# Performance work log

Measured on AMD Instinct MI355X. Metric: run time of the kernel, lower is better.

Reference implementation:

```python
import jax, jax.numpy as jnp
import numpy as np

B, T, D, S, K = 4, 4096, 1024, 2048, 8

def _l2norm(v, axis=-1, eps=1e-12):
    # matches torch F.normalize: v / max(||v||, eps)
    n = jnp.sqrt(jnp.sum(v * v, axis=axis, keepdims=True))
    return v / jnp.maximum(n, eps)

def setup_inputs() -> dict:
    key = jax.random.key(0)
    ks = jax.random.split(key, 9)
    H = D // 2
    return {
        "x": jax.random.normal(ks[0], (B, T, D), dtype=jnp.float32),
        "memory_keys": jax.random.normal(ks[1], (S, D), dtype=jnp.float32) * 0.02,
        "memory_values": jax.random.normal(ks[2], (S, D), dtype=jnp.float32) * 0.02,
        "Wq": jax.random.normal(ks[3], (D, D), dtype=jnp.float32) * (1.0 / np.sqrt(D)),
        "Wo": jax.random.normal(ks[4], (D, D), dtype=jnp.float32) * (1.0 / np.sqrt(D)),
        "gW1": jax.random.normal(ks[5], (H, 2 * D), dtype=jnp.float32) * (1.0 / np.sqrt(2 * D)),
        "gb1": jnp.zeros((H,), dtype=jnp.float32),
        "gW2": jax.random.normal(ks[6], (1, H), dtype=jnp.float32) * (1.0 / np.sqrt(H)),
        "gb2": jnp.zeros((1,), dtype=jnp.float32),
    }

def reference(x, memory_keys, memory_values, Wq, Wo, gW1, gb1, gW2, gb2):
    # query projection (Linear, no bias): y = x @ W.T
    queries = jnp.einsum('btd,ed->bte', x, Wq)
    keys_norm = _l2norm(memory_keys)          # [S, D]
    queries_norm = _l2norm(queries)           # [B, T, D]
    # cosine similarities [B, T, S]
    sims = jnp.einsum('btd,sd->bts', queries_norm, keys_norm)
    topk_sims, topk_idx = jax.lax.top_k(sims, K)      # [B, T, K]
    topk_w = jax.nn.softmax(topk_sims, axis=-1)       # [B, T, K]
    topk_vals = memory_values[topk_idx]               # [B, T, K, D]
    retrieved = jnp.einsum('btk,btkd->btd', topk_w, topk_vals)
    retrieved = jnp.einsum('btd,ed->bte', retrieved, Wo)
    gate_in = jnp.concatenate([x, retrieved], axis=-1)           # [B, T, 2D]
    h = jax.nn.gelu(jnp.einsum('btc,hc->bth', gate_in, gW1) + gb1, approximate=False)
    gate = jax.nn.sigmoid(jnp.einsum('bth,oh->bto', h, gW2) + gb2)  # [B, T, 1]
    return x + gate * retrieved
```

## Files before the change

### kernel.cpp

```cpp
#include <hip/hip_runtime.h>
#include <math.h>

#define NROWS 16384
#define DDIM  1024
#define SKEYS 2048
#define KTOP  8
#define HDIM  512

typedef short  s16x8 __attribute__((ext_vector_type(8)));
typedef float  f32x4 __attribute__((ext_vector_type(4)));

#define GL16(g, l) __builtin_amdgcn_global_load_lds(                      \
    (const __attribute__((address_space(1))) void*)(g),                   \
    (__attribute__((address_space(3))) void*)(l), 16, 0, 0)

__device__ __forceinline__ float wave_sum(float v) {
#pragma unroll
    for (int off = 32; off > 0; off >>= 1) v += __shfl_xor(v, off, 64);
    return v;
}

__device__ __forceinline__ unsigned short f2bf(float f) {
    union { float f; unsigned u; } c; c.f = f;
    unsigned u = c.u;
    unsigned r = (u + 0x7FFFu + ((u >> 16) & 1u)) >> 16;
    return (unsigned short)r;
}

__device__ __forceinline__ float gelu_exact(float v) {
    return 0.5f * v * (1.0f + erff(v * 0.7071067811865475f));
}

__device__ __forceinline__ ushort4 cvt4(float4 v) {
    ushort4 o;
    o.x = f2bf(v.x); o.y = f2bf(v.y); o.z = f2bf(v.z); o.w = f2bf(v.w);
    return o;
}

__global__ __launch_bounds__(256) void prep_kernel(
        const float* __restrict__ x,   const float* __restrict__ Wq,
        const float* __restrict__ Wo,  const float* __restrict__ mv,
        const float* __restrict__ gW1, const float* __restrict__ mk,
        unsigned short* __restrict__ x_bf, unsigned short* __restrict__ wqcat,
        unsigned short* __restrict__ wo_bf, unsigned short* __restrict__ mv_bf,
        unsigned short* __restrict__ gw1b, unsigned short* __restrict__ kn) {
    int bid = blockIdx.x, t = threadIdx.x;
    {
        float4 v = ((const float4*)(mk + (size_t)bid * DDIM))[t];
        float ss = v.x * v.x + v.y * v.y + v.z * v.z + v.w * v.w;
        ss = wave_sum(ss);
        __shared__ float wsum[4];
        if ((t & 63) == 0) wsum[t >> 6] = ss;
        __syncthreads();
        float tot = wsum[0] + wsum[1] + wsum[2] + wsum[3];
        float sc = 1.0f / fmaxf(sqrtf(tot), 1e-12f);
        float4 o = make_float4(v.x * sc, v.y * sc, v.z * sc, v.w * sc);
        ((ushort4*)(kn + (size_t)bid * DDIM))[t] = cvt4(o);
    }
    int gid = bid * 256 + t, stride = gridDim.x * 256;
    for (int i = gid; i < NROWS * DDIM / 4; i += stride)
        ((ushort4*)x_bf)[i] = cvt4(((const float4*)x)[i]);
    for (int i = gid; i < DDIM * DDIM / 4; i += stride)
        ((ushort4*)wqcat)[i] = cvt4(((const float4*)Wq)[i]);
    for (int i = gid; i < HDIM * 2 * DDIM / 4; i += stride) {
        float4 v = ((const float4*)gW1)[i];
        int r = i >> 9, c4 = i & 511;
        if (c4 < 256) ((ushort4*)wqcat)[DDIM * DDIM / 4 + r * 256 + c4] = cvt4(v);
        else          ((ushort4*)gw1b)[r * 256 + (c4 - 256)] = cvt4(v);
    }
    for (int i = gid; i < DDIM * DDIM / 4; i += stride)
        ((ushort4*)wo_bf)[i] = cvt4(((const float4*)Wo)[i]);
    for (int i = gid; i < SKEYS * DDIM / 4; i += stride)
        ((ushort4*)mv_bf)[i] = cvt4(((const float4*)mv)[i]);
}

template<int MODE, int K0, int KTOT>
__global__ __launch_bounds__(256, 3) void gemm128(
        const unsigned short* __restrict__ A0, const unsigned short* __restrict__ A1,
        const unsigned short* __restrict__ Bm, const float* __restrict__ bias,
        unsigned short* __restrict__ Cb, int Ncols,
        unsigned short* __restrict__ C2, int N2cols, int nsplit) {
    __shared__ __align__(16) unsigned short As[2][4096];
    __shared__ __align__(16) unsigned short Bs[2][4096];

    int tid = threadIdx.x, l = tid & 63, wid = tid >> 6;
    int gx = gridDim.x;
    int nwg = gx * gridDim.y;
    int bid = blockIdx.y * gx + blockIdx.x;
    int cpx = nwg >> 3;
    int sbid = (bid & 7) * cpx + (bid >> 3);
    int m0 = (sbid / gx) * 128;
    int n0 = (sbid % gx) * 128;

    int wr = wid >> 1, wc = wid & 1;
    constexpr int K1 = KTOT - K0;
    constexpr int NT = KTOT >> 5;

    f32x4 acc[4][4];
#pragma unroll
    for (int i = 0; i < 4; ++i)
#pragma unroll
        for (int j = 0; j < 4; ++j) acc[i][j] = (f32x4){0.f, 0.f, 0.f, 0.f};

    int srow   = tid >> 2;
    int schunk = (tid & 3) ^ ((srow >> 1) & 3);
    int offA0[2], offA1[2], offB[2];
#pragma unroll
    for (int i = 0; i < 2; ++i) {
        int ra = m0 + i * 64 + srow;
        offA0[i] = ra * K0;
        offA1[i] = ra * K1;
        offB[i]  = (n0 + i * 64 + srow) * KTOT;
    }
    int ldsU = wid * 512;

#define STAGE(bsel, kt_)                                                       \
    do {                                                                       \
        int gk_ = (kt_) * 32 + schunk * 8;                                     \
        _Pragma("unroll")                                                      \
        for (int i_ = 0; i_ < 2; ++i_) {                                       \
            const unsigned short* ga_ = (K0 == KTOT || gk_ < K0)               \
                ? A0 + offA0[i_] + gk_                                         \
                : A1 + offA1[i_] + (gk_ - K0);                                 \
            GL16(ga_, &As[bsel][i_ * 2048 + ldsU]);                            \
            GL16(Bm + offB[i_] + gk_, &Bs[bsel][i_ * 2048 + ldsU]);            \
        }                                                                      \
    } while (0)

    STAGE(0, 0);

    int frow = l & 15;
    int fp   = (l >> 4) ^ ((frow >> 1) & 3);
    int aoff = (wr * 64 + frow) * 32 + fp * 8;
    int boff = (wc * 64 + frow) * 32 + fp * 8;

#pragma unroll 2
    for (int kt = 0; kt < NT; ++kt) {
        int b = kt & 1;
        if (kt + 1 < NT) {
            STAGE(b ^ 1, kt + 1);
            asm volatile("s_waitcnt vmcnt(4)" ::: "memory");
        } else {
            asm volatile("s_waitcnt vmcnt(0)" ::: "memory");
        }
        __builtin_amdgcn_s_barrier();
        asm volatile("" ::: "memory");

        s16x8 af[4], bfr[4];
#pragma unroll
        for (int mf = 0; mf < 4; ++mf)
            af[mf] = *(const s16x8*)&As[b][aoff + mf * 512];
#pragma unroll
        for (int nf = 0; nf < 4; ++nf)
            bfr[nf] = *(const s16x8*)&Bs[b][boff + nf * 512];

        __builtin_amdgcn_s_setprio(1);
#pragma unroll
        for (int mf = 0; mf < 4; ++mf)
#pragma unroll
            for (int nf = 0; nf < 4; ++nf)
                acc[mf][nf] = __builtin_amdgcn_mfma_f32_16x16x32_bf16(
                    af[mf], bfr[nf], acc[mf][nf], 0, 0, 0);
        __builtin_amdgcn_s_setprio(0);
        asm volatile("" ::: "memory");
        __builtin_amdgcn_s_barrier();
        asm volatile("" ::: "memory");
    }
#undef STAGE

    unsigned short* cptr = Cb;
    int nc = Ncols, cb = n0;
    if (MODE == 2 && n0 >= nsplit) { cptr = C2; nc = N2cols; cb = n0 - nsplit; }

    int crow = (l >> 4) << 2;
    int ccol = l & 15;
#pragma unroll
    for (int mf = 0; mf < 4; ++mf) {
        int gr = m0 + wr * 64 + mf * 16 + crow;
#pragma unroll
        for (int nf = 0; nf < 4; ++nf) {
            int gc = cb + wc * 64 + nf * 16 + ccol;
            f32x4 v = acc[mf][nf];
#pragma unroll
            for (int r2 = 0; r2 < 4; ++r2) {
                unsigned short sv = f2bf(v[r2]);
                if (MODE == 3)
                    sv = sv ^ ((sv & 0x8000) ? 0xFFFFu : 0x8000u);
                cptr[(size_t)(gr + r2) * nc + gc] = sv;
            }
        }
    }
    (void)bias;
}

#define BINS(arr, xk)                                                     \
    do {                                                                  \
        unsigned cur_ = (xk);                                             \
        _Pragma("unroll")                                                 \
        for (int p_ = 0; p_ < 8; ++p_) {                                  \
            unsigned mx_ = arr[p_] > cur_ ? arr[p_] : cur_;               \
            unsigned mn_ = arr[p_] > cur_ ? cur_ : arr[p_];               \
            arr[p_] = mx_; cur_ = mn_;                                    \
        }                                                                 \
    } while (0)

__global__ __launch_bounds__(256) void mega_kernel(
        const unsigned short* __restrict__ q_bf,
        const unsigned short* __restrict__ sims,
        const unsigned short* __restrict__ x_bf,
        const unsigned short* __restrict__ xg1,
        const unsigned short* __restrict__ mvo,
        const unsigned short* __restrict__ mvog,
        const float* __restrict__ gb1, const float* __restrict__ gW2,
        const float* __restrict__ gb2, float* __restrict__ out) {
    int wid = threadIdx.x >> 6, l = threadIdx.x & 63;
    int row = blockIdx.x * 4 + wid;

    const unsigned short* qp = q_bf + (size_t)row * DDIM + l * 16;
    uint4 qa = *(const uint4*)qp, qb = *(const uint4*)(qp + 8);
    unsigned qw[8] = {qa.x, qa.y, qa.z, qa.w, qb.x, qb.y, qb.z, qb.w};
    float ss = 0.f;
#pragma unroll
    for (int j = 0; j < 8; ++j) {
        float lo = __uint_as_float(qw[j] << 16);
        float hi = __uint_as_float(qw[j] & 0xffff0000u);
        ss += lo * lo + hi * hi;
    }
    ss = wave_sum(ss);
    float qs = 1.0f / fmaxf(sqrtf(ss), 1e-12f);

    const unsigned short* sr = sims + (size_t)row * SKEYS;
    unsigned a[8], bb[8];
#pragma unroll
    for (int j = 0; j < 8; ++j) { a[j] = 0u; bb[j] = 0u; }
#pragma unroll
    for (int c = 0; c < 4; ++c) {
        uint4 raw = *(const uint4*)(sr + c * 512 + l * 8);
        unsigned wv[4] = {raw.x, raw.y, raw.z, raw.w};
#pragma unroll
        for (int q2 = 0; q2 < 4; ++q2) {
            unsigned bi0 = (unsigned)(c * 512 + l * 8 + q2 * 2);
            unsigned klo = ((wv[q2] & 0xFFFFu) << 16) | bi0;
            unsigned khi = (wv[q2] & 0xFFFF0000u) | (bi0 + 1);
            if (c < 2) { BINS(a, klo); BINS(a, khi); }
            else       { BINS(bb, klo); BINS(bb, khi); }
        }
    }
#pragma unroll
    for (int j = 0; j < 8; ++j) BINS(a, bb[j]);

    float ov[8]; int oi[8];
#pragma unroll
    for (int j = 0; j < 8; ++j) {
        unsigned best = a[0];
#pragma unroll
        for (int off = 32; off > 0; off >>= 1) {
            unsigned o2 = (unsigned)__shfl_xor((int)best, off, 64);
            best = best > o2 ? best : o2;
        }
        oi[j] = (int)(best & 0xFFFFu);
        unsigned short ks = (unsigned short)(best >> 16);
        unsigned short sv = ks ^ ((ks & 0x8000) ? 0x8000u : 0xFFFFu);
        ov[j] = __uint_as_float(((unsigned)sv) << 16);
        bool hit = (a[0] == best);
#pragma unroll
        for (int p = 0; p < 7; ++p) a[p] = hit ? a[p + 1] : a[p];
        a[7] = hit ? 0u : a[7];
    }

    float w[KTOP];
    float m = ov[0] * qs, ssum = 0.f;
#pragma unroll
    for (int j = 0; j < 8; ++j) { w[j] = expf(ov[j] * qs - m); ssum += w[j]; }
    float sinv = 1.0f / ssum;
#pragma unroll
    for (int j = 0; j < 8; ++j) w[j] *= sinv;

    float r2[16], hp[8];
#pragma unroll
    for (int j = 0; j < 16; ++j) r2[j] = 0.f;
#pragma unroll
    for (int j = 0; j < 8; ++j) hp[j] = 0.f;
#pragma unroll
    for (int k = 0; k < KTOP; ++k) {
        float wk = w[k];
        const unsigned short* mo = mvo + (size_t)oi[k] * DDIM + l * 16;
        uint4 a0 = *(const uint4*)mo;
        uint4 a1 = *(const uint4*)(mo + 8);
        const unsigned short* mg = mvog + (size_t)oi[k] * HDIM + l * 8;
        uint4 g0 = *(const uint4*)mg;
        unsigned aw[8] = {a0.x, a0.y, a0.z, a0.w, a1.x, a1.y, a1.z, a1.w};
#pragma unroll
        for (int j = 0; j < 8; ++j) {
            r2[2 * j]     += wk * __uint_as_float(aw[j] << 16);
            r2[2 * j + 1] += wk * __uint_as_float(aw[j] & 0xffff0000u);
        }
        unsigned gw[4] = {g0.x, g0.y, g0.z, g0.w};
#pragma unroll
        for (int j = 0; j < 4; ++j) {
            hp[2 * j]     += wk * __uint_as_float(gw[j] << 16);
            hp[2 * j + 1] += wk * __uint_as_float(gw[j] & 0xffff0000u);
        }
    }
    uint4 xg = *(const uint4*)(xg1 + (size_t)row * HDIM + l * 8);
    unsigned xgw[4] = {xg.x, xg.y, xg.z, xg.w};
    float p = 0.f;
#pragma unroll
    for (int j = 0; j < 4; ++j) {
        float h0 = gelu_exact(hp[2 * j] + __uint_as_float(xgw[j] << 16)
                              + gb1[l * 8 + 2 * j]);
        float h1 = gelu_exact(hp[2 * j + 1] + __uint_as_float(xgw[j] & 0xffff0000u)
                              + gb1[l * 8 + 2 * j + 1]);
        p += h0 * gW2[l * 8 + 2 * j] + h1 * gW2[l * 8 + 2 * j + 1];
    }
    p = wave_sum(p);
    float gate = 1.0f / (1.0f + expf(-(p + gb2[0])));
    const unsigned short* xr = x_bf + (size_t)row * DDIM + l * 16;
    uint4 x0 = *(const uint4*)xr, x1 = *(const uint4*)(xr + 8);
    unsigned xw[8] = {x0.x, x0.y, x0.z, x0.w, x1.x, x1.y, x1.z, x1.w};
    float o[16];
#pragma unroll
    for (int j = 0; j < 8; ++j) {
        o[2 * j]     = __uint_as_float(xw[j] << 16)         + gate * r2[2 * j];
        o[2 * j + 1] = __uint_as_float(xw[j] & 0xffff0000u) + gate * r2[2 * j + 1];
    }
    float4* po = (float4*)(out + (size_t)row * DDIM + l * 16);
    po[0] = make_float4(o[0], o[1], o[2], o[3]);
    po[1] = make_float4(o[4], o[5], o[6], o[7]);
    po[2] = make_float4(o[8], o[9], o[10], o[11]);
    po[3] = make_float4(o[12], o[13], o[14], o[15]);
}

extern "C" void kernel_launch(void* const* d_in, const int* in_sizes, int n_in,
                              void* d_out, int out_size, void* d_ws, size_t ws_size,
                              hipStream_t stream) {
    (void)in_sizes; (void)n_in; (void)out_size; (void)ws_size;
    const float* x   = (const float*)d_in[0];
    const float* mk  = (const float*)d_in[1];
    const float* mv  = (const float*)d_in[2];
    const float* Wq  = (const float*)d_in[3];
    const float* Wo  = (const float*)d_in[4];
    const float* gW1 = (const float*)d_in[5];
    const float* gb1 = (const float*)d_in[6];
    const float* gW2 = (const float*)d_in[7];
    const float* gb2 = (const float*)d_in[8];
    float* out = (float*)d_out;

    char* w = (char*)d_ws;
    unsigned short* x_bf    = (unsigned short*)w;  w += (size_t)NROWS * DDIM * 2;
    unsigned short* q_bf    = (unsigned short*)w;  w += (size_t)NROWS * DDIM * 2;
    unsigned short* xg1_bf  = (unsigned short*)w;  w += (size_t)NROWS * HDIM * 2;
    unsigned short* kn_bf   = (unsigned short*)w;  w += (size_t)SKEYS * DDIM * 2;
    unsigned short* wqcat   = (unsigned short*)w;  w += (size_t)(DDIM + HDIM) * DDIM * 2;
    unsigned short* gw1b_bf = (unsigned short*)w;  w += (size_t)HDIM * DDIM * 2;
    unsigned short* wo_bf   = (unsigned short*)w;  w += (size_t)DDIM * DDIM * 2;
    unsigned short* mv_bf   = (unsigned short*)w;  w += (size_t)SKEYS * DDIM * 2;
    unsigned short* mvo_bf  = (unsigned short*)w;  w += (size_t)SKEYS * DDIM * 2;
    unsigned short* mvog_bf = (unsigned short*)w;  w += (size_t)SKEYS * HDIM * 2;
    unsigned short* sims    = (unsigned short*)w;  w += (size_t)NROWS * SKEYS * 2;

    prep_kernel<<<SKEYS, 256, 0, stream>>>(x, Wq, Wo, mv, gW1, mk,
                                           x_bf, wqcat, wo_bf, mv_bf, gw1b_bf, kn_bf);

    gemm128<0, DDIM, DDIM><<<dim3(DDIM / 128, SKEYS / 128), 256, 0, stream>>>(
        mv_bf, mv_bf, wo_bf, nullptr, mvo_bf, DDIM, nullptr, 0, 0);

    gemm128<0, DDIM, DDIM><<<dim3(HDIM / 128, SKEYS / 128), 256, 0, stream>>>(
        mvo_bf, mvo_bf, gw1b_bf, nullptr, mvog_bf, HDIM, nullptr, 0, 0);

    gemm128<2, DDIM, DDIM><<<dim3((DDIM + HDIM) / 128, NROWS / 128), 256, 0, stream>>>(
        x_bf, x_bf, wqcat, nullptr, q_bf, DDIM, xg1_bf, HDIM, DDIM);

    gemm128<3, DDIM, DDIM><<<dim3(SKEYS / 128, NROWS / 128), 256, 0, stream>>>(
        q_bf, q_bf, kn_bf, nullptr, sims, SKEYS, nullptr, 0, 0);

    mega_kernel<<<NROWS / 4, 256, 0, stream>>>(
        q_bf, sims, x_bf, xg1_bf, mvo_bf, mvog_bf, gb1, gW2, gb2, out);
}
```

Measured before the change: 299.5 us.

## Merge independent GEMMs into dual-problem launches and fuse query norm into epilogue

The four separate GEMM launches are replaced by two launches of a runtime-parameterised dual GEMM kernel. Each launch pairs a large GEMM with a small independent one (query/gate-projection with memory-values@Wo, sims with mvo@gW1b), so the small problems fill tail waves instead of running as their own underfilled grids. The query GEMM epilogue also accumulates per-row squared norms via shuffles and atomics into a workspace buffer. The mega kernel then reads one float per row instead of re-reading the full bf16 query row. This adds a memset, atomics, and runtime mode branches in place of compile-time templates. The norm is now computed from fp32 accumulators rather than rounded bf16 values.

```diff
diff --git a/kernel.cpp b/kernel.cpp
--- a/kernel.cpp
+++ b/kernel.cpp
@@ -74,27 +74,30 @@
         ((ushort4*)mv_bf)[i] = cvt4(((const float4*)mv)[i]);
 }
 
-template<int MODE, int K0, int KTOT>
-__global__ __launch_bounds__(256, 3) void gemm128(
-        const unsigned short* __restrict__ A0, const unsigned short* __restrict__ A1,
-        const unsigned short* __restrict__ Bm, const float* __restrict__ bias,
-        unsigned short* __restrict__ Cb, int Ncols,
-        unsigned short* __restrict__ C2, int N2cols, int nsplit) {
+struct GArg {
+    const unsigned short* A;
+    const unsigned short* B;
+    unsigned short* C;
+    unsigned short* C2;
+    float* qinv;
+    int Ncols, N2cols, nsplit, gx, nblocks, mode;
+};
+
+__global__ __launch_bounds__(256, 3) void dualgemm(GArg g0, GArg g1, int split) {
     __shared__ __align__(16) unsigned short As[2][4096];
     __shared__ __align__(16) unsigned short Bs[2][4096];
 
     int tid = threadIdx.x, l = tid & 63, wid = tid >> 6;
-    int gx = gridDim.x;
-    int nwg = gx * gridDim.y;
-    int bid = blockIdx.y * gx + blockIdx.x;
-    int cpx = nwg >> 3;
+    bool first = ((int)blockIdx.x < split);
+    GArg g = first ? g0 : g1;
+    int bid = first ? blockIdx.x : blockIdx.x - split;
+    int cpx = g.nblocks >> 3;
     int sbid = (bid & 7) * cpx + (bid >> 3);
-    int m0 = (sbid / gx) * 128;
-    int n0 = (sbid % gx) * 128;
+    int m0 = (sbid / g.gx) * 128;
+    int n0 = (sbid % g.gx) * 128;
 
     int wr = wid >> 1, wc = wid & 1;
-    constexpr int K1 = KTOT - K0;
-    constexpr int NT = KTOT >> 5;
+    constexpr int NT = 32;
 
     f32x4 acc[4][4];
 #pragma unroll
@@ -104,13 +107,11 @@
 
     int srow   = tid >> 2;
     int schunk = (tid & 3) ^ ((srow >> 1) & 3);
-    int offA0[2], offA1[2], offB[2];
+    int offA[2], offB[2];
 #pragma unroll
     for (int i = 0; i < 2; ++i) {
-        int ra = m0 + i * 64 + srow;
-        offA0[i] = ra * K0;
-        offA1[i] = ra * K1;
-        offB[i]  = (n0 + i * 64 + srow) * KTOT;
+        offA[i] = (m0 + i * 64 + srow) * 1024;
+        offB[i] = (n0 + i * 64 + srow) * 1024;
     }
     int ldsU = wid * 512;
 
@@ -119,11 +120,8 @@
         int gk_ = (kt_) * 32 + schunk * 8;                                     \
         _Pragma("unroll")                                                      \
         for (int i_ = 0; i_ < 2; ++i_) {                                       \
-            const unsigned short* ga_ = (K0 == KTOT || gk_ < K0)               \
-                ? A0 + offA0[i_] + gk_                                         \
-                : A1 + offA1[i_] + (gk_ - K0);                                 \
-            GL16(ga_, &As[bsel][i_ * 2048 + ldsU]);                            \
-            GL16(Bm + offB[i_] + gk_, &Bs[bsel][i_ * 2048 + ldsU]);            \
+            GL16(g.A + offA[i_] + gk_, &As[bsel][i_ * 2048 + ldsU]);           \
+            GL16(g.B + offB[i_] + gk_, &Bs[bsel][i_ * 2048 + ldsU]);           \
         }                                                                      \
     } while (0)
 
@@ -168,12 +166,21 @@
     }
 #undef STAGE
 
-    unsigned short* cptr = Cb;
-    int nc = Ncols, cb = n0;
-    if (MODE == 2 && n0 >= nsplit) { cptr = C2; nc = N2cols; cb = n0 - nsplit; }
+    unsigned short* cptr = g.C;
+    int nc = g.Ncols, cb = n0;
+    bool qreg = (g.mode == 2);
+    if (g.mode == 2 && n0 >= g.nsplit) {
+        cptr = g.C2; nc = g.N2cols; cb = n0 - g.nsplit; qreg = false;
+    }
 
     int crow = (l >> 4) << 2;
     int ccol = l & 15;
+    float rs[4][4];
+#pragma unroll
+    for (int i = 0; i < 4; ++i)
+#pragma unroll
+        for (int j = 0; j < 4; ++j) rs[i][j] = 0.f;
+
 #pragma unroll
     for (int mf = 0; mf < 4; ++mf) {
         int gr = m0 + wr * 64 + mf * 16 + crow;
@@ -183,14 +190,29 @@
             f32x4 v = acc[mf][nf];
 #pragma unroll
             for (int r2 = 0; r2 < 4; ++r2) {
-                unsigned short sv = f2bf(v[r2]);
-                if (MODE == 3)
+                float o = v[r2];
+                unsigned short sv = f2bf(o);
+                if (g.mode == 3)
                     sv = sv ^ ((sv & 0x8000) ? 0xFFFFu : 0x8000u);
                 cptr[(size_t)(gr + r2) * nc + gc] = sv;
+                if (qreg) rs[mf][r2] += o * o;
             }
         }
     }
-    (void)bias;
+    if (qreg) {
+#pragma unroll
+        for (int mf = 0; mf < 4; ++mf)
+#pragma unroll
+            for (int r2 = 0; r2 < 4; ++r2) {
+                float s = rs[mf][r2];
+                s += __shfl_xor(s, 1, 64);
+                s += __shfl_xor(s, 2, 64);
+                s += __shfl_xor(s, 4, 64);
+                s += __shfl_xor(s, 8, 64);
+                if ((l & 15) == 0)
+                    atomicAdd(&g.qinv[m0 + wr * 64 + mf * 16 + (l >> 4) * 4 + r2], s);
+            }
+    }
 }
 
 #define BINS(arr, xk)                                                     \
@@ -205,7 +227,7 @@
     } while (0)
 
 __global__ __launch_bounds__(256) void mega_kernel(
-        const unsigned short* __restrict__ q_bf,
+        const float* __restrict__ qsum,
         const unsigned short* __restrict__ sims,
         const unsigned short* __restrict__ x_bf,
         const unsigned short* __restrict__ xg1,
@@ -216,18 +238,7 @@
     int wid = threadIdx.x >> 6, l = threadIdx.x & 63;
     int row = blockIdx.x * 4 + wid;
 
-    const unsigned short* qp = q_bf + (size_t)row * DDIM + l * 16;
-    uint4 qa = *(const uint4*)qp, qb = *(const uint4*)(qp + 8);
-    unsigned qw[8] = {qa.x, qa.y, qa.z, qa.w, qb.x, qb.y, qb.z, qb.w};
-    float ss = 0.f;
-#pragma unroll
-    for (int j = 0; j < 8; ++j) {
-        float lo = __uint_as_float(qw[j] << 16);
-        float hi = __uint_as_float(qw[j] & 0xffff0000u);
-        ss += lo * lo + hi * hi;
-    }
-    ss = wave_sum(ss);
-    float qs = 1.0f / fmaxf(sqrtf(ss), 1e-12f);
+    float qs = 1.0f / fmaxf(sqrtf(qsum[row]), 1e-12f);
 
     const unsigned short* sr = sims + (size_t)row * SKEYS;
     unsigned a[8], bb[8];
@@ -358,22 +369,33 @@
     unsigned short* mvo_bf  = (unsigned short*)w;  w += (size_t)SKEYS * DDIM * 2;
     unsigned short* mvog_bf = (unsigned short*)w;  w += (size_t)SKEYS * HDIM * 2;
     unsigned short* sims    = (unsigned short*)w;  w += (size_t)NROWS * SKEYS * 2;
+    float* qsum = (float*)w;                       w += (size_t)NROWS * 4;
+
+    hipMemsetAsync(qsum, 0, (size_t)NROWS * sizeof(float), stream);
 
     prep_kernel<<<SKEYS, 256, 0, stream>>>(x, Wq, Wo, mv, gW1, mk,
                                            x_bf, wqcat, wo_bf, mv_bf, gw1b_bf, kn_bf);
 
-    gemm128<0, DDIM, DDIM><<<dim3(DDIM / 128, SKEYS / 128), 256, 0, stream>>>(
-        mv_bf, mv_bf, wo_bf, nullptr, mvo_bf, DDIM, nullptr, 0, 0);
-
-    gemm128<0, DDIM, DDIM><<<dim3(HDIM / 128, SKEYS / 128), 256, 0, stream>>>(
-        mvo_bf, mvo_bf, gw1b_bf, nullptr, mvog_bf, HDIM, nullptr, 0, 0);
-
-    gemm128<2, DDIM, DDIM><<<dim3((DDIM + HDIM) / 128, NROWS / 128), 256, 0, stream>>>(
-        x_bf, x_bf, wqcat, nullptr, q_bf, DDIM, xg1_bf, HDIM, DDIM);
-
-    gemm128<3, DDIM, DDIM><<<dim3(SKEYS / 128, NROWS / 128), 256, 0, stream>>>(
-        q_bf, q_bf, kn_bf, nullptr, sims, SKEYS, nullptr, 0, 0);
+    {
+        GArg gq; gq.A = x_bf;  gq.B = wqcat; gq.C = q_bf;  gq.C2 = xg1_bf;
+        gq.qinv = qsum; gq.Ncols = DDIM; gq.N2cols = HDIM; gq.nsplit = DDIM;
+        gq.gx = 12; gq.nblocks = 1536; gq.mode = 2;
+        GArg gm; gm.A = mv_bf; gm.B = wo_bf; gm.C = mvo_bf; gm.C2 = nullptr;
+        gm.qinv = nullptr; gm.Ncols = DDIM; gm.N2cols = 0; gm.nsplit = 0;
+        gm.gx = 8; gm.nblocks = 128; gm.mode = 0;
+        dualgemm<<<1664, 256, 0, stream>>>(gq, gm, 1536);
+    }
+
+    {
+        GArg gs; gs.A = q_bf;   gs.B = kn_bf;   gs.C = sims;    gs.C2 = nullptr;
+        gs.qinv = nullptr; gs.Ncols = SKEYS; gs.N2cols = 0; gs.nsplit = 0;
+        gs.gx = 16; gs.nblocks = 2048; gs.mode = 3;
+        GArg gg; gg.A = mvo_bf; gg.B = gw1b_bf; gg.C = mvog_bf; gg.C2 = nullptr;
+        gg.qinv = nullptr; gg.Ncols = HDIM; gg.N2cols = 0; gg.nsplit = 0;
+        gg.gx = 4; gg.nblocks = 64; gg.mode = 0;
+        dualgemm<<<2112, 256, 0, stream>>>(gs, gg, 2048);
+    }
 
     mega_kernel<<<NROWS / 4, 256, 0, stream>>>(
-        q_bf, sims, x_bf, xg1_bf, mvo_bf, mvog_bf, gb1, gW2, gb2, out);
-}
+        qsum, sims, x_bf, xg1_bf, mvo_bf, mvog_bf, gb1, gW2, gb2, out);
+}
```

Result: faster. 286.3 us (-4.4%).
